# Performance work log

Measured on AMD Instinct MI355X. Metric: run time of the kernel, lower is better.

The kernel has to match this reference:

```python
import jax, jax.numpy as jnp
from jax import lax
import numpy as np

K = 3        # adaptive kernel size
STRIDE = 1
PAD = (K - 1) // 2


def setup_inputs() -> dict:
    key = jax.random.key(0)
    ks = jax.random.split(key, 10)
    N, C, H, W = 32, 512, 56, 56
    Cm, P = 128, 512  # Cm = inplanes // m, P = planes

    def rn(k, shape, scale=0.05):
        return jax.random.normal(k, shape, dtype=jnp.float32) * scale

    return dict(
        x=jax.random.normal(ks[0], (N, C, H, W), dtype=jnp.float32),
        conv_w=rn(ks[1], (Cm, C)),      # self.conv 1x1 weight (squeezed)
        conv_b=rn(ks[2], (Cm,)),        # self.conv bias
        ck_w=rn(ks[3], (K * K,)),       # self.conv_kernel 1x1 weight (1 in-ch)
        ck_b=rn(ks[4], (K * K,)),       # self.conv_kernel bias
        ckk_w=rn(ks[5], (Cm,)),         # self.conv_k 1x1 weight (1 in-ch)
        ckk_b=rn(ks[6], (Cm,)),         # self.conv_k bias
        adap_b=rn(ks[7], (Cm,)),        # self.conv_adap_kernel bias (weight is generated)
        fuse_w=rn(ks[8], (P, Cm)),      # self.fuse 1x1 weight (squeezed)
        fuse_b=rn(ks[9], (P,)),         # self.fuse bias
    )


def _forward(x, conv_w, conv_b, ck_w, ck_b, ckk_w, ckk_b, adap_b, fuse_w, fuse_b):
    N, C, H, W = x.shape
    Cm = conv_w.shape[0]

    # f = relu(conv(x)) : [N, Cm, H, W]
    f = jax.nn.relu(jnp.einsum('nchw,oc->nohw', x, conv_w) + conv_b[None, :, None, None])

    # g = relu(conv(avg_pool(x))) : [N, Cm]  (spatial dims are 1x1, squeezed)
    pooled = jnp.mean(x, axis=(2, 3))                       # [N, C]
    g = jax.nn.relu(pooled @ conv_w.T + conv_b)             # [N, Cm]

    # conv_kernel (1x1, 1->k*k channels) applied on permuted g:
    # ker[n, ic, kk] = ck_w[kk] * g[n, ic] + ck_b[kk]
    ker = g[:, :, None] * ck_w[None, None, :] + ck_b[None, None, :]   # [N, Cm, k*k]

    # conv_k (1x1, 1->Cm channels) generates per-sample dynamic conv weights:
    # Wk[n, oc, ic, kk] = relu(ckk_w[oc] * ker[n, ic, kk] + ckk_b[oc])
    Wk = jax.nn.relu(ckk_w[None, :, None, None] * ker[:, None, :, :]
                     + ckk_b[None, :, None, None])          # [N, Cm, Cm, k*k]
    Wk = Wk.reshape(N, Cm, Cm, K, K)                        # per-sample OIHW weights

    # Per-sample dynamic conv, batched with vmap (replaces the python loop + weight swap)
    def dyn_conv(f_n, w_n):  # f_n: [Cm,H,W], w_n: [Cm,Cm,K,K]
        return lax.conv_general_dilated(
            f_n[None], w_n, (STRIDE, STRIDE), [(PAD, PAD), (PAD, PAD)],
            dimension_numbers=('NCHW', 'OIHW', 'NCHW'))[0]

    y = jax.vmap(dyn_conv)(f, Wk) + adap_b[None, :, None, None]  # [N, Cm, H, W]

    # fuse 1x1 conv: Cm -> planes
    out = jnp.einsum('nchw,pc->nphw', y, fuse_w) + fuse_b[None, :, None, None]
    return out


def reference(x, conv_w, conv_b, ck_w, ck_b, ckk_w, ckk_b, adap_b, fuse_w, fuse_b):
    return _forward(x, conv_w, conv_b, ck_w, ck_b, ckk_w, ckk_b, adap_b, fuse_w, fuse_b)
```

## Files before the change

### kernel.cpp

```cpp
#include <hip/hip_runtime.h>

#define N_   32
#define C_   512
#define HW_  3136
#define W_   56
#define H_   56
#define CM_  128
#define P_   512

typedef __attribute__((ext_vector_type(8))) short bf16x8;
typedef __attribute__((ext_vector_type(4))) float f32x4;

__device__ inline ushort f2bf(float x) {
    unsigned u = __float_as_uint(x);
    u += 0x7fff + ((u >> 16) & 1);
    return (ushort)(u >> 16);
}

__global__ __launch_bounds__(256) void prep_w(const float* __restrict__ conv_w,
                                              const float* __restrict__ fuse_w,
                                              ushort* __restrict__ Acv,
                                              ushort* __restrict__ Afu) {
    int idx = blockIdx.x * 256 + threadIdx.x;
    if (idx < 65536) {
        int ci = idx & 7, cm = (idx >> 3) & 127, cb = idx >> 10;
        Acv[idx] = f2bf(conv_w[cm * C_ + cb * 8 + ci]);
    } else {
        int j = idx - 65536;
        int ci = j & 7, p = (j >> 3) & 511, kb = j >> 12;
        Afu[j] = f2bf(fuse_w[p * CM_ + kb * 8 + ci]);
    }
}

__global__ __launch_bounds__(256) void gemm_f(const float* __restrict__ x,
                                              const ushort* __restrict__ Acv,
                                              const float* __restrict__ conv_b,
                                              ushort* __restrict__ f_t,
                                              float* __restrict__ gacc) {
    int pixbase = blockIdx.x * 64, n = blockIdx.z;
    int t = threadIdx.x, wv = t >> 6, lane = t & 63, col = lane & 15, quad = lane >> 4;
    __shared__ ushort bsh[2][64 * 40];
    f32x4 z = {0.f, 0.f, 0.f, 0.f};
    f32x4 acc[2][4];
    #pragma unroll
    for (int mt = 0; mt < 2; mt++)
        #pragma unroll
        for (int ns = 0; ns < 4; ns++) acc[mt][ns] = z;

    int spix = t >> 2, chq = (t & 3) * 8;
    const float* xb = &x[(size_t)n * C_ * HW_ + pixbase + spix];

    float v[8];
#define LOADV(c0)                                                              \
    {                                                                          \
        const float* xs = xb + (size_t)(c0) * HW_;                             \
        _Pragma("unroll")                                                      \
        for (int i = 0; i < 8; i++) v[i] = xs[(size_t)(chq + i) * HW_];        \
    }
#define PACKW(buf)                                                             \
    {                                                                          \
        unsigned p0 = (unsigned)f2bf(v[0]) | ((unsigned)f2bf(v[1]) << 16);     \
        unsigned p1 = (unsigned)f2bf(v[2]) | ((unsigned)f2bf(v[3]) << 16);     \
        unsigned p2 = (unsigned)f2bf(v[4]) | ((unsigned)f2bf(v[5]) << 16);     \
        unsigned p3 = (unsigned)f2bf(v[6]) | ((unsigned)f2bf(v[7]) << 16);     \
        *(uint4*)&bsh[buf][spix * 40 + chq] = make_uint4(p0, p1, p2, p3);      \
    }

    LOADV(0);
    PACKW(0);
    __syncthreads();
    int cur = 0;
    for (int cb0 = 0; cb0 < 16; cb0++) {
        if (cb0 < 15) {
            LOADV((cb0 + 1) * 32);
            PACKW(cur ^ 1);
        }
        bf16x8 a[2], b[4];
        #pragma unroll
        for (int mt = 0; mt < 2; mt++)
            a[mt] = *(const bf16x8*)&Acv[(((cb0 * 4 + quad) * CM_) + wv * 32 + mt * 16 + col) * 8];
        #pragma unroll
        for (int ns = 0; ns < 4; ns++)
            b[ns] = *(const bf16x8*)&bsh[cur][(ns * 16 + col) * 40 + quad * 8];
        #pragma unroll
        for (int mt = 0; mt < 2; mt++)
            #pragma unroll
            for (int ns = 0; ns < 4; ns++)
                acc[mt][ns] = __builtin_amdgcn_mfma_f32_16x16x32_bf16(a[mt], b[ns], acc[mt][ns], 0, 0, 0);
        __syncthreads();
        cur ^= 1;
    }
#undef LOADV
#undef PACKW

    #pragma unroll
    for (int mt = 0; mt < 2; mt++) {
        float ps0 = acc[mt][0][0] + acc[mt][1][0] + acc[mt][2][0] + acc[mt][3][0];
        float ps1 = acc[mt][0][1] + acc[mt][1][1] + acc[mt][2][1] + acc[mt][3][1];
        float ps2 = acc[mt][0][2] + acc[mt][1][2] + acc[mt][2][2] + acc[mt][3][2];
        float ps3 = acc[mt][0][3] + acc[mt][1][3] + acc[mt][2][3] + acc[mt][3][3];
        #pragma unroll
        for (int off = 1; off < 16; off <<= 1) {
            ps0 += __shfl_xor(ps0, off);
            ps1 += __shfl_xor(ps1, off);
            ps2 += __shfl_xor(ps2, off);
            ps3 += __shfl_xor(ps3, off);
        }
        if (col == 0) {
            int ocr = wv * 32 + mt * 16 + quad * 4;
            atomicAdd(&gacc[n * CM_ + ocr],     ps0);
            atomicAdd(&gacc[n * CM_ + ocr + 1], ps1);
            atomicAdd(&gacc[n * CM_ + ocr + 2], ps2);
            atomicAdd(&gacc[n * CM_ + ocr + 3], ps3);
        }
    }

    #pragma unroll
    for (int mt = 0; mt < 2; mt++) {
        int ocr = wv * 32 + mt * 16 + quad * 4;
        float b0 = conv_b[ocr], b1 = conv_b[ocr + 1], b2 = conv_b[ocr + 2], b3 = conv_b[ocr + 3];
        #pragma unroll
        for (int ns = 0; ns < 4; ns++) {
            int pix = pixbase + ns * 16 + col;
            ushort4 o;
            o.x = f2bf(fmaxf(acc[mt][ns][0] + b0, 0.f));
            o.y = f2bf(fmaxf(acc[mt][ns][1] + b1, 0.f));
            o.z = f2bf(fmaxf(acc[mt][ns][2] + b2, 0.f));
            o.w = f2bf(fmaxf(acc[mt][ns][3] + b3, 0.f));
            *(ushort4*)&f_t[((size_t)(n * HW_ + pix)) * CM_ + ocr] = o;
        }
    }
}

__global__ __launch_bounds__(256) void wk_frag(const float* __restrict__ gacc,
                                               const float* __restrict__ conv_b,
                                               const float* __restrict__ ck_w,
                                               const float* __restrict__ ck_b,
                                               const float* __restrict__ ckk_w,
                                               const float* __restrict__ ckk_b,
                                               ushort* __restrict__ Wkf) {
    int idx = blockIdx.x * 256 + threadIdx.x;
    int ci = idx & 7, oc = (idx >> 3) & 127, icb = (idx >> 10) & 15, rest = idx >> 14;
    int kk = rest % 9, n = rest / 9;
    int ic = icb * 8 + ci;
    float gv = fmaxf(gacc[n * CM_ + ic] * (1.0f / (float)HW_) + conv_b[ic], 0.f);
    float ker = ck_w[kk] * gv + ck_b[kk];
    Wkf[idx] = f2bf(fmaxf(ckk_w[oc] * ker + ckk_b[oc], 0.f));
}

__global__ __launch_bounds__(256) void gemm_dyn(const ushort* __restrict__ f_t,
                                                const ushort* __restrict__ Wkf,
                                                const float* __restrict__ adap_b,
                                                ushort* __restrict__ y_t) {
    int pixbase = blockIdx.x * 64, n = blockIdx.z;
    int t = threadIdx.x, wv = t >> 6, lane = t & 63, col = lane & 15, quad = lane >> 4;
    int h_lo = pixbase / W_;
    __shared__ ushort fsh[232 * 40];
    int ldspix[4];
    #pragma unroll
    for (int ns = 0; ns < 4; ns++) {
        int pix = pixbase + ns * 16 + col;
        int h = pix / W_, w = pix - h * W_;
        ldspix[ns] = (h - h_lo) * 58 + w;
    }
    f32x4 acc[2][4];
    #pragma unroll
    for (int mt = 0; mt < 2; mt++) {
        int ocr = wv * 32 + mt * 16 + quad * 4;
        f32x4 ab = {adap_b[ocr], adap_b[ocr + 1], adap_b[ocr + 2], adap_b[ocr + 3]};
        #pragma unroll
        for (int ns = 0; ns < 4; ns++) acc[mt][ns] = ab;
    }
    for (int ic0 = 0; ic0 < CM_; ic0 += 32) {
        #pragma unroll
        for (int it = 0; it < 4; it++) {
            int idx = it * 256 + t;
            if (idx < 928) {
                int lp = idx >> 2, ch = idx & 3;
                int r = lp / 58, cw = lp - r * 58;
                int hp = h_lo + r;
                uint4 v = {0u, 0u, 0u, 0u};
                if (hp >= 1 && hp <= H_ && cw >= 1 && cw <= W_)
                    v = *(const uint4*)&f_t[((size_t)(n * HW_ + (hp - 1) * W_ + cw - 1)) * CM_ + ic0 + ch * 8];
                *(uint4*)&fsh[lp * 40 + ch * 8] = v;
            }
        }
        __syncthreads();
        #pragma unroll
        for (int dh = 0; dh < 3; dh++) {
            #pragma unroll
            for (int dw = 0; dw < 3; dw++) {
                int kk = dh * 3 + dw;
                bf16x8 a[2], b[4];
                #pragma unroll
                for (int mt = 0; mt < 2; mt++)
                    a[mt] = *(const bf16x8*)&Wkf[((((size_t)(n * 9 + kk) * 16) + (ic0 >> 3) + quad) * CM_ + wv * 32 + mt * 16 + col) * 8];
                #pragma unroll
                for (int ns = 0; ns < 4; ns++)
                    b[ns] = *(const bf16x8*)&fsh[(ldspix[ns] + dh * 58 + dw) * 40 + quad * 8];
                #pragma unroll
                for (int mt = 0; mt < 2; mt++)
                    #pragma unroll
                    for (int ns = 0; ns < 4; ns++)
                        acc[mt][ns] = __builtin_amdgcn_mfma_f32_16x16x32_bf16(a[mt], b[ns], acc[mt][ns], 0, 0, 0);
            }
        }
        __syncthreads();
    }
    #pragma unroll
    for (int mt = 0; mt < 2; mt++) {
        int ocr = wv * 32 + mt * 16 + quad * 4;
        #pragma unroll
        for (int ns = 0; ns < 4; ns++) {
            int pix = pixbase + ns * 16 + col;
            ushort4 o;
            o.x = f2bf(acc[mt][ns][0]);
            o.y = f2bf(acc[mt][ns][1]);
            o.z = f2bf(acc[mt][ns][2]);
            o.w = f2bf(acc[mt][ns][3]);
            *(ushort4*)&y_t[((size_t)(n * HW_ + pix)) * CM_ + ocr] = o;
        }
    }
}

__global__ __launch_bounds__(256) void gemm_fuse(const ushort* __restrict__ y_t,
                                                 const ushort* __restrict__ Afu,
                                                 const float* __restrict__ fuse_b,
                                                 float* __restrict__ out) {
    int pixbase = blockIdx.x * 64, pbase = blockIdx.y * 128, n = blockIdx.z;
    int t = threadIdx.x, wv = t >> 6, lane = t & 63, col = lane & 15, quad = lane >> 4;
    __shared__ ushort bsh[64 * 40];
    f32x4 z = {0.f, 0.f, 0.f, 0.f};
    f32x4 acc[2][4];
    #pragma unroll
    for (int mt = 0; mt < 2; mt++)
        #pragma unroll
        for (int ns = 0; ns < 4; ns++) acc[mt][ns] = z;
    int spix = t >> 2, sch = t & 3;
    const ushort* srcbase = &y_t[((size_t)(n * HW_ + pixbase + spix)) * CM_ + sch * 8];
    for (int cb0 = 0; cb0 < 4; cb0++) {
        *(uint4*)&bsh[spix * 40 + sch * 8] = *(const uint4*)(srcbase + cb0 * 32);
        __syncthreads();
        bf16x8 a[2], b[4];
        #pragma unroll
        for (int mt = 0; mt < 2; mt++)
            a[mt] = *(const bf16x8*)&Afu[(((cb0 * 4 + quad) * P_) + pbase + wv * 32 + mt * 16 + col) * 8];
        #pragma unroll
        for (int ns = 0; ns < 4; ns++)
            b[ns] = *(const bf16x8*)&bsh[(ns * 16 + col) * 40 + quad * 8];
        #pragma unroll
        for (int mt = 0; mt < 2; mt++)
            #pragma unroll
            for (int ns = 0; ns < 4; ns++)
                acc[mt][ns] = __builtin_amdgcn_mfma_f32_16x16x32_bf16(a[mt], b[ns], acc[mt][ns], 0, 0, 0);
        __syncthreads();
    }
    #pragma unroll
    for (int mt = 0; mt < 2; mt++) {
        int pr = pbase + wv * 32 + mt * 16 + quad * 4;
        #pragma unroll
        for (int ns = 0; ns < 4; ns++) {
            int pix = pixbase + ns * 16 + col;
            #pragma unroll
            for (int r = 0; r < 4; r++)
                out[((size_t)(n * P_ + pr + r)) * HW_ + pix] = acc[mt][ns][r] + fuse_b[pr + r];
        }
    }
}

extern "C" void kernel_launch(void* const* d_in, const int* in_sizes, int n_in,
                              void* d_out, int out_size, void* d_ws, size_t ws_size,
                              hipStream_t stream) {
    const float* x      = (const float*)d_in[0];
    const float* conv_w = (const float*)d_in[1];
    const float* conv_b = (const float*)d_in[2];
    const float* ck_w   = (const float*)d_in[3];
    const float* ck_b   = (const float*)d_in[4];
    const float* ckk_w  = (const float*)d_in[5];
    const float* ckk_b  = (const float*)d_in[6];
    const float* adap_b = (const float*)d_in[7];
    const float* fuse_w = (const float*)d_in[8];
    const float* fuse_b = (const float*)d_in[9];
    float* out = (float*)d_out;

    ushort* y_t = (ushort*)d_ws;
    ushort* f_t = y_t + (size_t)12845056;
    ushort* Wkf = f_t + (size_t)12845056;
    ushort* Acv = Wkf + (size_t)4718592;
    ushort* Afu = Acv + (size_t)65536;
    float* gacc = (float*)(Afu + (size_t)65536);

    hipMemsetAsync(gacc, 0, 4096 * sizeof(float), stream);
    prep_w<<<512, 256, 0, stream>>>(conv_w, fuse_w, Acv, Afu);
    gemm_f<<<dim3(49, 1, N_), 256, 0, stream>>>(x, Acv, conv_b, f_t, gacc);
    wk_frag<<<18432, 256, 0, stream>>>(gacc, conv_b, ck_w, ck_b, ckk_w, ckk_b, Wkf);
    gemm_dyn<<<dim3(49, 1, N_), 256, 0, stream>>>(f_t, Wkf, adap_b, y_t);
    gemm_fuse<<<dim3(49, 4, N_), 256, 0, stream>>>(y_t, Afu, fuse_b, out);
}
```

Measured before the change: 463.8 us.

## Fuse dynamic conv with fuse 1x1 GEMM via shared memory, fold memset into prep

Merges the dynamic 3x3 conv kernel and the final 1x1 fuse GEMM. The bf16 y tile stays in shared memory and is consumed directly for all four output-channel blocks, so y is never written to or read back from global memory. It also zeroes the gacc accumulator inside prep_w instead of issuing a separate memset. The cost is extra LDS per block, which may lower occupancy, and the fuse GEMM runs serially inside 1568 blocks instead of being spread over 6272 blocks.

Measured after the change: 451.4 us. -2.7%, faster.

```diff
diff --git a/kernel.cpp b/kernel.cpp
--- a/kernel.cpp
+++ b/kernel.cpp
@@ -20,8 +20,10 @@
 __global__ __launch_bounds__(256) void prep_w(const float* __restrict__ conv_w,
                                               const float* __restrict__ fuse_w,
                                               ushort* __restrict__ Acv,
-                                              ushort* __restrict__ Afu) {
+                                              ushort* __restrict__ Afu,
+                                              float* __restrict__ gacc) {
     int idx = blockIdx.x * 256 + threadIdx.x;
+    if (idx < 4096) gacc[idx] = 0.f;
     if (idx < 65536) {
         int ci = idx & 7, cm = (idx >> 3) & 127, cb = idx >> 10;
         Acv[idx] = f2bf(conv_w[cm * C_ + cb * 8 + ci]);
@@ -148,14 +150,17 @@
     Wkf[idx] = f2bf(fmaxf(ckk_w[oc] * ker + ckk_b[oc], 0.f));
 }
 
-__global__ __launch_bounds__(256) void gemm_dyn(const ushort* __restrict__ f_t,
-                                                const ushort* __restrict__ Wkf,
-                                                const float* __restrict__ adap_b,
-                                                ushort* __restrict__ y_t) {
+__global__ __launch_bounds__(256) void gemm_dyn_fuse(const ushort* __restrict__ f_t,
+                                                     const ushort* __restrict__ Wkf,
+                                                     const float* __restrict__ adap_b,
+                                                     const ushort* __restrict__ Afu,
+                                                     const float* __restrict__ fuse_b,
+                                                     float* __restrict__ out) {
     int pixbase = blockIdx.x * 64, n = blockIdx.z;
     int t = threadIdx.x, wv = t >> 6, lane = t & 63, col = lane & 15, quad = lane >> 4;
     int h_lo = pixbase / W_;
     __shared__ ushort fsh[232 * 40];
+    __shared__ ushort ysh[4][64 * 40];
     int ldspix[4];
     #pragma unroll
     for (int ns = 0; ns < 4; ns++) {
@@ -207,63 +212,55 @@
         }
         __syncthreads();
     }
-    #pragma unroll
-    for (int mt = 0; mt < 2; mt++) {
-        int ocr = wv * 32 + mt * 16 + quad * 4;
+
+    #pragma unroll
+    for (int mt = 0; mt < 2; mt++) {
         #pragma unroll
         for (int ns = 0; ns < 4; ns++) {
-            int pix = pixbase + ns * 16 + col;
+            int lpix = ns * 16 + col;
             ushort4 o;
             o.x = f2bf(acc[mt][ns][0]);
             o.y = f2bf(acc[mt][ns][1]);
             o.z = f2bf(acc[mt][ns][2]);
             o.w = f2bf(acc[mt][ns][3]);
-            *(ushort4*)&y_t[((size_t)(n * HW_ + pix)) * CM_ + ocr] = o;
-        }
-    }
-}
-
-__global__ __launch_bounds__(256) void gemm_fuse(const ushort* __restrict__ y_t,
-                                                 const ushort* __restrict__ Afu,
-                                                 const float* __restrict__ fuse_b,
-                                                 float* __restrict__ out) {
-    int pixbase = blockIdx.x * 64, pbase = blockIdx.y * 128, n = blockIdx.z;
-    int t = threadIdx.x, wv = t >> 6, lane = t & 63, col = lane & 15, quad = lane >> 4;
-    __shared__ ushort bsh[64 * 40];
-    f32x4 z = {0.f, 0.f, 0.f, 0.f};
-    f32x4 acc[2][4];
-    #pragma unroll
-    for (int mt = 0; mt < 2; mt++)
-        #pragma unroll
-        for (int ns = 0; ns < 4; ns++) acc[mt][ns] = z;
-    int spix = t >> 2, sch = t & 3;
-    const ushort* srcbase = &y_t[((size_t)(n * HW_ + pixbase + spix)) * CM_ + sch * 8];
-    for (int cb0 = 0; cb0 < 4; cb0++) {
-        *(uint4*)&bsh[spix * 40 + sch * 8] = *(const uint4*)(srcbase + cb0 * 32);
-        __syncthreads();
-        bf16x8 a[2], b[4];
+            *(ushort4*)&ysh[wv][lpix * 40 + mt * 16 + quad * 4] = o;
+        }
+    }
+    __syncthreads();
+
+    #pragma unroll 1
+    for (int pb = 0; pb < 4; pb++) {
+        f32x4 z = {0.f, 0.f, 0.f, 0.f};
+        f32x4 facc[2][4];
         #pragma unroll
         for (int mt = 0; mt < 2; mt++)
-            a[mt] = *(const bf16x8*)&Afu[(((cb0 * 4 + quad) * P_) + pbase + wv * 32 + mt * 16 + col) * 8];
-        #pragma unroll
-        for (int ns = 0; ns < 4; ns++)
-            b[ns] = *(const bf16x8*)&bsh[(ns * 16 + col) * 40 + quad * 8];
-        #pragma unroll
-        for (int mt = 0; mt < 2; mt++)
+            #pragma unroll
+            for (int ns = 0; ns < 4; ns++) facc[mt][ns] = z;
+        #pragma unroll
+        for (int cb0 = 0; cb0 < 4; cb0++) {
+            bf16x8 a[2], b[4];
+            #pragma unroll
+            for (int mt = 0; mt < 2; mt++)
+                a[mt] = *(const bf16x8*)&Afu[(((cb0 * 4 + quad) * P_) + pb * 128 + wv * 32 + mt * 16 + col) * 8];
             #pragma unroll
             for (int ns = 0; ns < 4; ns++)
-                acc[mt][ns] = __builtin_amdgcn_mfma_f32_16x16x32_bf16(a[mt], b[ns], acc[mt][ns], 0, 0, 0);
-        __syncthreads();
-    }
-    #pragma unroll
-    for (int mt = 0; mt < 2; mt++) {
-        int pr = pbase + wv * 32 + mt * 16 + quad * 4;
-        #pragma unroll
-        for (int ns = 0; ns < 4; ns++) {
-            int pix = pixbase + ns * 16 + col;
-            #pragma unroll
-            for (int r = 0; r < 4; r++)
-                out[((size_t)(n * P_ + pr + r)) * HW_ + pix] = acc[mt][ns][r] + fuse_b[pr + r];
+                b[ns] = *(const bf16x8*)&ysh[cb0][(ns * 16 + col) * 40 + quad * 8];
+            #pragma unroll
+            for (int mt = 0; mt < 2; mt++)
+                #pragma unroll
+                for (int ns = 0; ns < 4; ns++)
+                    facc[mt][ns] = __builtin_amdgcn_mfma_f32_16x16x32_bf16(a[mt], b[ns], facc[mt][ns], 0, 0, 0);
+        }
+        #pragma unroll
+        for (int mt = 0; mt < 2; mt++) {
+            int pr = pb * 128 + wv * 32 + mt * 16 + quad * 4;
+            #pragma unroll
+            for (int ns = 0; ns < 4; ns++) {
+                int pix = pixbase + ns * 16 + col;
+                #pragma unroll
+                for (int r = 0; r < 4; r++)
+                    out[((size_t)(n * P_ + pr + r)) * HW_ + pix] = facc[mt][ns][r] + fuse_b[pr + r];
+            }
         }
     }
 }
@@ -283,17 +280,14 @@
     const float* fuse_b = (const float*)d_in[9];
     float* out = (float*)d_out;
 
-    ushort* y_t = (ushort*)d_ws;
-    ushort* f_t = y_t + (size_t)12845056;
+    ushort* f_t = (ushort*)d_ws;
     ushort* Wkf = f_t + (size_t)12845056;
     ushort* Acv = Wkf + (size_t)4718592;
     ushort* Afu = Acv + (size_t)65536;
     float* gacc = (float*)(Afu + (size_t)65536);
 
-    hipMemsetAsync(gacc, 0, 4096 * sizeof(float), stream);
-    prep_w<<<512, 256, 0, stream>>>(conv_w, fuse_w, Acv, Afu);
+    prep_w<<<512, 256, 0, stream>>>(conv_w, fuse_w, Acv, Afu, gacc);
     gemm_f<<<dim3(49, 1, N_), 256, 0, stream>>>(x, Acv, conv_b, f_t, gacc);
     wk_frag<<<18432, 256, 0, stream>>>(gacc, conv_b, ck_w, ck_b, ckk_w, ckk_b, Wkf);
-    gemm_dyn<<<dim3(49, 1, N_), 256, 0, stream>>>(f_t, Wkf, adap_b, y_t);
-    gemm_fuse<<<dim3(49, 4, N_), 256, 0, stream>>>(y_t, Afu, fuse_b, out);
-}
+    gemm_dyn_fuse<<<dim3(49, 1, N_), 256, 0, stream>>>(f_t, Wkf, adap_b, Afu, fuse_b, out);
+}
```
